# Performance work log

Measured on AMD Instinct MI355X. Metric: run time of the kernel, lower is better.

Reference implementation:

```python
import jax, jax.numpy as jnp
import numpy as np

N_NODES = 50000
N_EDGES = 640000
HID = 128
EDGE_FEAT = 4
NUM_G = 20
R_MIN, R_MAX = 0.0, 10.0

def setup_inputs() -> dict:
    key = jax.random.key(0)
    ks = jax.random.split(key, 16)
    s = lambda d: 1.0 / np.sqrt(d)
    return {
        'h': jax.random.normal(ks[0], (N_NODES, HID), jnp.float32),
        'x': jax.random.normal(ks[1], (N_NODES, 3), jnp.float32),
        'edge_index': jax.random.randint(ks[2], (2, N_EDGES), 0, N_NODES, dtype=jnp.int64),
        'mask_ligand': jnp.ones((N_NODES,), jnp.float32),
        'edge_attr': jax.random.normal(ks[3], (N_EDGES, EDGE_FEAT), jnp.float32),
        'We1': jax.random.normal(ks[4], (2*HID+EDGE_FEAT+NUM_G, HID), jnp.float32) * s(2*HID+EDGE_FEAT+NUM_G),
        'be1': jnp.zeros((HID,), jnp.float32),
        'We2': jax.random.normal(ks[5], (HID, HID), jnp.float32) * s(HID),
        'be2': jnp.zeros((HID,), jnp.float32),
        'Winf': jax.random.normal(ks[6], (HID, 1), jnp.float32) * s(HID),
        'binf': jnp.zeros((1,), jnp.float32),
        'Wx1': jax.random.normal(ks[7], (HID, HID), jnp.float32) * s(HID),
        'bx1': jnp.zeros((HID,), jnp.float32),
        'Wx2': jax.random.normal(ks[8], (HID, 1), jnp.float32) * 0.001 * s(HID),
        'Wn1': jax.random.normal(ks[9], (2*HID, HID), jnp.float32) * s(2*HID),
        'bn1': jnp.zeros((HID,), jnp.float32),
        'Wn2': jax.random.normal(ks[10], (HID, HID), jnp.float32) * s(HID),
        'bn2': jnp.zeros((HID,), jnp.float32),
    }

def reference(h, x, edge_index, mask_ligand, edge_attr,
              We1, be1, We2, be2, Winf, binf, Wx1, bx1, Wx2, Wn1, bn1, Wn2, bn2):
    n = h.shape[0]
    src, dst = edge_index[0], edge_index[1]
    hi, hj = h[dst], h[src]                      # [E, H] gathers
    rel_x = x[dst] - x[src]                      # [E, 3]
    d_sq = jnp.sum(rel_x**2, axis=-1, keepdims=True)  # [E, 1]
    d = jnp.sqrt(d_sq + 1e-8)
    # GaussianSmearing(r_min=0, r_max=10, num_gaussians=20)
    offset = jnp.linspace(R_MIN, R_MAX, NUM_G, dtype=h.dtype)
    coeff = -0.5 / (offset[1] - offset[0])**2
    d_feat = jnp.exp(coeff * (d - offset)**2)    # [E, 20]
    edge_feat = jnp.concatenate([d_feat, edge_attr], axis=-1)
    # edge MLP (2 layers, silu, act_last=True)
    z = jnp.concatenate([hi, hj, edge_feat], axis=-1)
    mij = jax.nn.silu(jax.nn.silu(z @ We1 + be1) @ We2 + be2)  # [E, H]
    eij = jax.nn.sigmoid(mij @ Winf + binf)      # [E, 1]
    mi = jax.ops.segment_sum(mij * eij, dst, num_segments=n)   # [N, H]
    # node MLP (2 layers, silu, no act on last)
    nz = jnp.concatenate([mi, h], axis=-1)
    h_out = h + (jax.nn.silu(nz @ Wn1 + bn1) @ Wn2 + bn2)
    # coordinate update
    xg = jnp.tanh(jax.nn.silu(mij @ Wx1 + bx1) @ Wx2)          # [E, 1]
    delta_x = jax.ops.segment_sum(rel_x / (d + 1.0) * xg, dst, num_segments=n)
    x_out = x + delta_x * mask_ligand[:, None]
    return h_out, x_out
```

## Files before the change

kernel.cpp:

```cpp
#include <hip/hip_runtime.h>
#include <math.h>

#define NN 50000
#define NE 640000
#define H 128
#define EPB 64
#define NPB 32
#define ZB 296
#define BB 136
#define KP1 288
#define NZB 264
#define NBPAD 50176
#define HISTB (NE / 256)
#define CONVB 464
#define ALLOCB (NBPAD / 256)
#define HCONVB 3125

typedef __attribute__((ext_vector_type(8))) unsigned short u16x8;
typedef __attribute__((ext_vector_type(8))) __bf16 bf16x8;
typedef __attribute__((ext_vector_type(2))) __bf16 bf16x2;
typedef __attribute__((ext_vector_type(4))) float f32x4;

__device__ __forceinline__ float frcp(float x) {
#if __has_builtin(__builtin_amdgcn_rcpf)
    return __builtin_amdgcn_rcpf(x);
#else
    return 1.0f / x;
#endif
}

__device__ __forceinline__ float silu_f(float v) {
    return v * frcp(1.0f + __expf(-v));
}

__device__ __forceinline__ float sigmoid_f(float v) {
    return frcp(1.0f + __expf(-v));
}

__device__ __forceinline__ float tanh_f(float v) {
    return 1.0f - 2.0f * frcp(1.0f + __expf(2.0f * v));
}

__device__ __forceinline__ unsigned short f2bf(float f) {
    unsigned int u = __builtin_bit_cast(unsigned int, f);
    u += 0x7FFFu + ((u >> 16) & 1u);
    return (unsigned short)(u >> 16);
}

__device__ __forceinline__ float bf2f(unsigned short s) {
    unsigned int u = ((unsigned int)s) << 16;
    return __builtin_bit_cast(float, u);
}

__device__ __forceinline__ unsigned int pkbf(float lo, float hi) {
#if __has_builtin(__builtin_amdgcn_cvt_pk_bf16_f32)
    bf16x2 v = __builtin_amdgcn_cvt_pk_bf16_f32(lo, hi);
    unsigned int r; __builtin_memcpy(&r, &v, 4); return r;
#else
    return (unsigned int)f2bf(lo) | ((unsigned int)f2bf(hi) << 16);
#endif
}

__device__ __forceinline__ f32x4 mfma16(u16x8 a, u16x8 b, f32x4 c) {
    return __builtin_amdgcn_mfma_f32_16x16x32_bf16(
        __builtin_bit_cast(bf16x8, a), __builtin_bit_cast(bf16x8, b), c, 0, 0, 0);
}

template<int KT, int INSTR, bool SYNC_BEFORE_EPI>
__device__ __forceinline__ void layer_mfma(
    const unsigned short* __restrict__ inbuf,
    const unsigned short* __restrict__ wt,
    const float* __restrict__ bias,
    unsigned short* __restrict__ outbuf,
    int wv, int quad, int r16)
{
    f32x4 acc[2][2] = {};
    const int F = wv * 32;
    #pragma unroll
    for (int ks = 0; ks < KT / 32; ks++) {
        int ko = ks * 32 + quad * 8;
        u16x8 b0 = *(const u16x8*)(inbuf + r16 * INSTR + ko);
        u16x8 b1 = *(const u16x8*)(inbuf + (16 + r16) * INSTR + ko);
        u16x8 a0 = *(const u16x8*)(wt + (size_t)(F + r16) * KT + ko);
        u16x8 a1 = *(const u16x8*)(wt + (size_t)(F + 16 + r16) * KT + ko);
        acc[0][0] = mfma16(a0, b0, acc[0][0]);
        acc[0][1] = mfma16(a0, b1, acc[0][1]);
        acc[1][0] = mfma16(a1, b0, acc[1][0]);
        acc[1][1] = mfma16(a1, b1, acc[1][1]);
    }
    if (SYNC_BEFORE_EPI) __syncthreads();
    #pragma unroll
    for (int rt = 0; rt < 2; rt++) {
        int f0 = F + rt * 16 + quad * 4;
        float4 bv = *(const float4*)(bias + f0);
        #pragma unroll
        for (int ci = 0; ci < 2; ci++) {
            int e = ci * 16 + r16;
            float s0 = silu_f(acc[rt][ci][0] + bv.x);
            float s1 = silu_f(acc[rt][ci][1] + bv.y);
            float s2 = silu_f(acc[rt][ci][2] + bv.z);
            float s3 = silu_f(acc[rt][ci][3] + bv.w);
            uint2 p = { pkbf(s0, s1), pkbf(s2, s3) };
            *(uint2*)(outbuf + e * BB + f0) = p;
        }
    }
}

__global__ __launch_bounds__(256) void init_kernel(
    float4* __restrict__ out4, int n4out,
    float4* __restrict__ ws4, int n4ws)
{
    int i = blockIdx.x * 256 + threadIdx.x;
    float4 z = make_float4(0.f, 0.f, 0.f, 0.f);
    if (i < n4out) out4[i] = z;
    else if (i - n4out < n4ws) ws4[i - n4out] = z;
}

__global__ __launch_bounds__(256) void hist_conv_kernel(
    const int* __restrict__ ei, int* __restrict__ cnt, int histBlocks,
    const float* __restrict__ We1, const float* __restrict__ We2,
    const float* __restrict__ Wx1, const float* __restrict__ Wn1,
    const float* __restrict__ Wn2,
    unsigned short* __restrict__ w1t, unsigned short* __restrict__ w2t,
    unsigned short* __restrict__ wx1t, unsigned short* __restrict__ wn1t,
    unsigned short* __restrict__ wn2t)
{
    int b = blockIdx.x, t = threadIdx.x;
    if (b < histBlocks) {
        int i = b * 256 + t;
        atomicAdd(&cnt[ei[NE + i]], 1);
        return;
    }
    int i = (b - histBlocks) * 256 + t;
    const int S1 = 128 * KP1;
    const int S2 = 128 * 128;
    const int S3 = 128 * 256;
    if (i < S1) {
        int n = i / KP1, k = i % KP1;
        w1t[i] = (k < 280) ? f2bf(We1[k * H + n]) : (unsigned short)0;
    } else if (i < S1 + S2) {
        int j = i - S1; int n = j / H, k = j % H;
        w2t[j] = f2bf(We2[k * H + n]);
    } else if (i < S1 + 2 * S2) {
        int j = i - S1 - S2; int n = j / H, k = j % H;
        wx1t[j] = f2bf(Wx1[k * H + n]);
    } else if (i < S1 + 2 * S2 + S3) {
        int j = i - S1 - 2 * S2; int n = j / 256, k = j % 256;
        wn1t[j] = f2bf(Wn1[k * H + n]);
    } else if (i < S1 + 3 * S2 + S3) {
        int j = i - S1 - 2 * S2 - S3; int n = j / H, k = j % H;
        wn2t[j] = f2bf(Wn2[k * H + n]);
    }
}

__global__ __launch_bounds__(256) void alloc_hconv_kernel(
    const int* __restrict__ cnt, int* __restrict__ cur, int* __restrict__ gtot,
    const float* __restrict__ h, unsigned short* __restrict__ hb,
    int allocBlocks)
{
    int b = blockIdx.x, t = threadIdx.x;
    if (b < allocBlocks) {
        int d = b * 256 + t;
        int v = cnt[d];
        int incl = v;
        #pragma unroll
        for (int o = 1; o < 64; o <<= 1) {
            int u = __shfl_up(incl, o, 64);
            if ((t & 63) >= o) incl += u;
        }
        int total = __shfl(incl, 63, 64);
        int base = 0;
        if ((t & 63) == 63) base = atomicAdd(gtot, total);
        base = __shfl(base, 63, 64);
        cur[d] = base + incl - v;
        return;
    }
    int j = (b - allocBlocks) * 256 + t;
    const float4* hp = (const float4*)h + (size_t)j * 2;
    float4 a = hp[0], c = hp[1];
    uint4 pk = { pkbf(a.x, a.y), pkbf(a.z, a.w), pkbf(c.x, c.y), pkbf(c.z, c.w) };
    ((uint4*)hb)[j] = pk;
}

__global__ __launch_bounds__(256) void scatter_kernel(
    const int* __restrict__ ei, const float* __restrict__ edge_attr,
    int* __restrict__ cur, uint4* __restrict__ epay)
{
    int i = blockIdx.x * 256 + threadIdx.x;
    int s = ei[i], d = ei[NE + i];
    float4 ea = ((const float4*)edge_attr)[i];
    int p = atomicAdd(&cur[d], 1);
    uint4 pv = { (unsigned)s, (unsigned)d, pkbf(ea.x, ea.y), pkbf(ea.z, ea.w) };
    epay[p] = pv;
}

__global__ __launch_bounds__(512, 6) void edge_kernel(
    const float* __restrict__ h, const float* __restrict__ x,
    const int* __restrict__ ei, const float* __restrict__ edge_attr,
    const unsigned short* __restrict__ w1t, const float* __restrict__ be1,
    const unsigned short* __restrict__ w2t, const float* __restrict__ be2,
    const float* __restrict__ Winf, const float* __restrict__ binf,
    const unsigned short* __restrict__ wx1t, const float* __restrict__ bx1,
    const float* __restrict__ Wx2,
    const uint4* __restrict__ epay, const unsigned short* __restrict__ hb,
    float* __restrict__ mi, float* __restrict__ dx)
{
    __shared__ unsigned short zs[EPB * ZB];
    __shared__ float relx_s[EPB][3];
    __shared__ float eij_s[EPB];
    __shared__ float xg_s[EPB];
    __shared__ float epart[8][EPB];
    __shared__ float xpart[8][EPB];
    __shared__ int dst_s[EPB];
    __shared__ float winf_s[H];
    __shared__ float wx2_s[H];

    unsigned short* m1 = zs;
    unsigned short* m2 = zs + EPB * BB;

    const int t = threadIdx.x;
    const int e0 = blockIdx.x * EPB;
    const bool srt = (epay != nullptr);

    if (t >= 128 && t < 256) {
        winf_s[t - 128] = Winf[t - 128];
        wx2_s[t - 128] = Wx2[t - 128];
    }

    {
        int e = t >> 3, l = t & 7;
        unsigned short* zr = zs + e * ZB;
        if (srt) {
            uint4 pv = epay[e0 + e];
            const uint4* hd = (const uint4*)(hb + (size_t)pv.y * H);
            const uint4* hs = (const uint4*)(hb + (size_t)pv.x * H);
            uint4 a0 = hd[l * 2], a1 = hd[l * 2 + 1];
            *(uint4*)(zr + l * 16) = a0;
            *(uint4*)(zr + l * 16 + 8) = a1;
            uint4 c0 = hs[l * 2], c1 = hs[l * 2 + 1];
            *(uint4*)(zr + 128 + l * 16) = c0;
            *(uint4*)(zr + 128 + l * 16 + 8) = c1;
        } else {
            int s = ei[e0 + e], d = ei[NE + e0 + e];
            const float4* hd = (const float4*)(h + (size_t)d * H);
            const float4* hs = (const float4*)(h + (size_t)s * H);
            float4 v0 = hd[l * 4 + 0], v1 = hd[l * 4 + 1];
            float4 v2 = hd[l * 4 + 2], v3 = hd[l * 4 + 3];
            uint4 p0 = { pkbf(v0.x, v0.y), pkbf(v0.z, v0.w), pkbf(v1.x, v1.y), pkbf(v1.z, v1.w) };
            uint4 p1 = { pkbf(v2.x, v2.y), pkbf(v2.z, v2.w), pkbf(v3.x, v3.y), pkbf(v3.z, v3.w) };
            *(uint4*)(zr + l * 16) = p0;
            *(uint4*)(zr + l * 16 + 8) = p1;
            float4 w0 = hs[l * 4 + 0], w1 = hs[l * 4 + 1];
            float4 w2 = hs[l * 4 + 2], w3 = hs[l * 4 + 3];
            uint4 q0 = { pkbf(w0.x, w0.y), pkbf(w0.z, w0.w), pkbf(w1.x, w1.y), pkbf(w1.z, w1.w) };
            uint4 q1 = { pkbf(w2.x, w2.y), pkbf(w2.z, w2.w), pkbf(w3.x, w3.y), pkbf(w3.z, w3.w) };
            *(uint4*)(zr + 128 + l * 16) = q0;
            *(uint4*)(zr + 128 + l * 16 + 8) = q1;
        }
    }
    if (t < EPB) {
        unsigned short* zr = zs + t * ZB;
        int s, d;
        if (srt) {
            uint4 pv = epay[e0 + t];
            s = (int)pv.x; d = (int)pv.y;
            *(unsigned int*)(zr + 276) = pv.z;
            *(unsigned int*)(zr + 278) = pv.w;
        } else {
            s = ei[e0 + t]; d = ei[NE + e0 + t];
            #pragma unroll
            for (int j = 0; j < 4; j++)
                zr[276 + j] = f2bf(edge_attr[(size_t)(e0 + t) * 4 + j]);
        }
        dst_s[t] = d;
        float rx = x[d * 3 + 0] - x[s * 3 + 0];
        float ry = x[d * 3 + 1] - x[s * 3 + 1];
        float rz = x[d * 3 + 2] - x[s * 3 + 2];
        float d2 = rx * rx + ry * ry + rz * rz;
        float dd = sqrtf(d2 + 1e-8f);
        float inv = frcp(dd + 1.0f);
        relx_s[t][0] = rx * inv;
        relx_s[t][1] = ry * inv;
        relx_s[t][2] = rz * inv;
        const float step = 10.0f / 19.0f;
        const float coeff = -0.5f / (step * step);
        #pragma unroll
        for (int g = 0; g < 20; g++) {
            float df = dd - step * (float)g;
            zr[256 + g] = f2bf(__expf(coeff * df * df));
        }
        #pragma unroll
        for (int j = 280; j < ZB; j++) zr[j] = 0;
    }
    __syncthreads();

    const int wv = t >> 6, lane = t & 63;
    const int quad = lane >> 4, r16 = lane & 15;
    const int F = wv * 16;
    const int f0 = F + quad * 4;

    {
        f32x4 acc[4] = {};
        #pragma unroll
        for (int ks = 0; ks < KP1 / 32; ks++) {
            int ko = ks * 32 + quad * 8;
            u16x8 a = *(const u16x8*)(w1t + (size_t)(F + r16) * KP1 + ko);
            #pragma unroll
            for (int ci = 0; ci < 4; ci++) {
                u16x8 b = *(const u16x8*)(zs + (ci * 16 + r16) * ZB + ko);
                acc[ci] = mfma16(a, b, acc[ci]);
            }
        }
        __syncthreads();
        float4 bv = *(const float4*)(be1 + f0);
        #pragma unroll
        for (int ci = 0; ci < 4; ci++) {
            int e = ci * 16 + r16;
            float s0 = silu_f(acc[ci][0] + bv.x);
            float s1 = silu_f(acc[ci][1] + bv.y);
            float s2 = silu_f(acc[ci][2] + bv.z);
            float s3 = silu_f(acc[ci][3] + bv.w);
            uint2 p = { pkbf(s0, s1), pkbf(s2, s3) };
            *(uint2*)(m1 + e * BB + f0) = p;
        }
    }
    __syncthreads();

    {
        f32x4 acc[4] = {};
        #pragma unroll
        for (int ks = 0; ks < H / 32; ks++) {
            int ko = ks * 32 + quad * 8;
            u16x8 a = *(const u16x8*)(w2t + (size_t)(F + r16) * H + ko);
            #pragma unroll
            for (int ci = 0; ci < 4; ci++) {
                u16x8 b = *(const u16x8*)(m1 + (ci * 16 + r16) * BB + ko);
                acc[ci] = mfma16(a, b, acc[ci]);
            }
        }
        float4 bv = *(const float4*)(be2 + f0);
        float4 wf = *(const float4*)(winf_s + f0);
        float ep[4];
        #pragma unroll
        for (int ci = 0; ci < 4; ci++) {
            int e = ci * 16 + r16;
            float s0 = silu_f(acc[ci][0] + bv.x);
            float s1 = silu_f(acc[ci][1] + bv.y);
            float s2 = silu_f(acc[ci][2] + bv.z);
            float s3 = silu_f(acc[ci][3] + bv.w);
            ep[ci] = s0 * wf.x + s1 * wf.y + s2 * wf.z + s3 * wf.w;
            uint2 p = { pkbf(s0, s1), pkbf(s2, s3) };
            *(uint2*)(m2 + e * BB + f0) = p;
        }
        #pragma unroll
        for (int ci = 0; ci < 4; ci++) {
            ep[ci] += __shfl_xor(ep[ci], 16, 64);
            ep[ci] += __shfl_xor(ep[ci], 32, 64);
        }
        if (quad == 0) {
            #pragma unroll
            for (int ci = 0; ci < 4; ci++)
                epart[wv][ci * 16 + r16] = ep[ci];
        }
    }
    __syncthreads();

    if (t < EPB) {
        float s = binf[0];
        #pragma unroll
        for (int w = 0; w < 8; w++) s += epart[w][t];
        eij_s[t] = sigmoid_f(s);
    }

    {
        f32x4 acc[4] = {};
        #pragma unroll
        for (int ks = 0; ks < H / 32; ks++) {
            int ko = ks * 32 + quad * 8;
            u16x8 a = *(const u16x8*)(wx1t + (size_t)(F + r16) * H + ko);
            #pragma unroll
            for (int ci = 0; ci < 4; ci++) {
                u16x8 b = *(const u16x8*)(m2 + (ci * 16 + r16) * BB + ko);
                acc[ci] = mfma16(a, b, acc[ci]);
            }
        }
        float4 bv = *(const float4*)(bx1 + f0);
        float4 wf = *(const float4*)(wx2_s + f0);
        float xp[4];
        #pragma unroll
        for (int ci = 0; ci < 4; ci++) {
            xp[ci] = silu_f(acc[ci][0] + bv.x) * wf.x
                   + silu_f(acc[ci][1] + bv.y) * wf.y
                   + silu_f(acc[ci][2] + bv.z) * wf.z
                   + silu_f(acc[ci][3] + bv.w) * wf.w;
        }
        #pragma unroll
        for (int ci = 0; ci < 4; ci++) {
            xp[ci] += __shfl_xor(xp[ci], 16, 64);
            xp[ci] += __shfl_xor(xp[ci], 32, 64);
        }
        if (quad == 0) {
            #pragma unroll
            for (int ci = 0; ci < 4; ci++)
                xpart[wv][ci * 16 + r16] = xp[ci];
        }
    }
    __syncthreads();

    if (t < EPB) {
        float xs = 0.f;
        #pragma unroll
        for (int w = 0; w < 8; w++) xs += xpart[w][t];
        xg_s[t] = tanh_f(xs);
    }
    __syncthreads();

    if (t < 128) {
        const int k = t;
        float acc = 0.f;
        int rs = 0;
        #pragma unroll
        for (int c = 0; c < EPB; c += 8) {
            float v[8];
            #pragma unroll
            for (int j = 0; j < 8; j++)
                v[j] = bf2f(m2[(c + j) * BB + k]) * eij_s[c + j];
            #pragma unroll
            for (int j = 0; j < 8; j++) {
                int e = c + j;
                acc += v[j];
                if (e == EPB - 1 || dst_s[e + 1] != dst_s[e]) {
                    float* p = &mi[(size_t)dst_s[e] * H + k];
                    if (srt && rs > 0 && e < EPB - 1) *p = acc;
                    else atomicAdd(p, acc);
                    acc = 0.f;
                    rs = e + 1;
                }
            }
        }
    } else if (t < 131) {
        const int dd = t - 128;
        float acc = 0.f;
        int rs = 0;
        #pragma unroll
        for (int c = 0; c < EPB; c += 8) {
            float v[8];
            #pragma unroll
            for (int j = 0; j < 8; j++)
                v[j] = relx_s[c + j][dd] * xg_s[c + j];
            #pragma unroll
            for (int j = 0; j < 8; j++) {
                int e = c + j;
                acc += v[j];
                if (e == EPB - 1 || dst_s[e + 1] != dst_s[e]) {
                    float* p = &dx[(size_t)dst_s[e] * 3 + dd];
                    if (srt && rs > 0 && e < EPB - 1) *p = acc;
                    else atomicAdd(p, acc);
                    acc = 0.f;
                    rs = e + 1;
                }
            }
        }
    }
}

__global__ __launch_bounds__(256, 8) void node_kernel(
    const float* __restrict__ h, const float* __restrict__ x,
    const float* __restrict__ mask,
    const unsigned short* __restrict__ wn1t, const float* __restrict__ bn1,
    const unsigned short* __restrict__ wn2t, const float* __restrict__ bn2,
    float* __restrict__ mi_hout, float* __restrict__ dx_xout)
{
    __shared__ unsigned short nzs[NPB * NZB];

    unsigned short* nbuf = nzs;

    const int t = threadIdx.x;
    const int n0 = blockIdx.x * NPB;

    {
        int r = t >> 3, l = t & 7;
        int n = n0 + r;
        unsigned short* zr = nzs + r * NZB;
        if (n < NN) {
            const float4* mi4 = (const float4*)(mi_hout + (size_t)n * H);
            const float4* h4  = (const float4*)(h + (size_t)n * H);
            float4 v0 = mi4[l * 4 + 0], v1 = mi4[l * 4 + 1];
            float4 v2 = mi4[l * 4 + 2], v3 = mi4[l * 4 + 3];
            uint4 p0 = { pkbf(v0.x, v0.y), pkbf(v0.z, v0.w), pkbf(v1.x, v1.y), pkbf(v1.z, v1.w) };
            uint4 p1 = { pkbf(v2.x, v2.y), pkbf(v2.z, v2.w), pkbf(v3.x, v3.y), pkbf(v3.z, v3.w) };
            *(uint4*)(zr + l * 16) = p0;
            *(uint4*)(zr + l * 16 + 8) = p1;
            float4 w0 = h4[l * 4 + 0], w1 = h4[l * 4 + 1];
            float4 w2 = h4[l * 4 + 2], w3 = h4[l * 4 + 3];
            uint4 q0 = { pkbf(w0.x, w0.y), pkbf(w0.z, w0.w), pkbf(w1.x, w1.y), pkbf(w1.z, w1.w) };
            uint4 q1 = { pkbf(w2.x, w2.y), pkbf(w2.z, w2.w), pkbf(w3.x, w3.y), pkbf(w3.z, w3.w) };
            *(uint4*)(zr + 128 + l * 16) = q0;
            *(uint4*)(zr + 128 + l * 16 + 8) = q1;
        } else {
            uint4 zf = {0u, 0u, 0u, 0u};
            *(uint4*)(zr + l * 16) = zf;
            *(uint4*)(zr + l * 16 + 8) = zf;
            *(uint4*)(zr + 128 + l * 16) = zf;
            *(uint4*)(zr + 128 + l * 16 + 8) = zf;
        }
    }

    float xo = 0.f;
    int xn = -1, xdim = 0;
    if (t < NPB * 3) {
        int r = t / 3; xdim = t % 3;
        int n = n0 + r;
        if (n < NN) {
            xn = n;
            xo = x[(size_t)n * 3 + xdim] + dx_xout[(size_t)n * 3 + xdim] * mask[n];
        }
    }
    __syncthreads();

    if (xn >= 0) dx_xout[(size_t)xn * 3 + xdim] = xo;

    const int wv = t >> 6, lane = t & 63;
    const int quad = lane >> 4, r16 = lane & 15;

    layer_mfma<2 * H, NZB, true>(nzs, wn1t, bn1, nbuf, wv, quad, r16);
    __syncthreads();

    {
        f32x4 acc[2][2] = {};
        const int F = wv * 32;
        #pragma unroll
        for (int ks = 0; ks < H / 32; ks++) {
            int ko = ks * 32 + quad * 8;
            u16x8 b0 = *(const u16x8*)(nbuf + r16 * BB + ko);
            u16x8 b1 = *(const u16x8*)(nbuf + (16 + r16) * BB + ko);
            u16x8 a0 = *(const u16x8*)(wn2t + (size_t)(F + r16) * H + ko);
            u16x8 a1 = *(const u16x8*)(wn2t + (size_t)(F + 16 + r16) * H + ko);
            acc[0][0] = mfma16(a0, b0, acc[0][0]);
            acc[0][1] = mfma16(a0, b1, acc[0][1]);
            acc[1][0] = mfma16(a1, b0, acc[1][0]);
            acc[1][1] = mfma16(a1, b1, acc[1][1]);
        }
        #pragma unroll
        for (int rt = 0; rt < 2; rt++) {
            int f0 = F + rt * 16 + quad * 4;
            float4 bv = *(const float4*)(bn2 + f0);
            #pragma unroll
            for (int ci = 0; ci < 2; ci++) {
                int n = n0 + ci * 16 + r16;
                if (n < NN) {
                    float4 hv = *(const float4*)(h + (size_t)n * H + f0);
                    float4 o;
                    o.x = hv.x + acc[rt][ci][0] + bv.x;
                    o.y = hv.y + acc[rt][ci][1] + bv.y;
                    o.z = hv.z + acc[rt][ci][2] + bv.z;
                    o.w = hv.w + acc[rt][ci][3] + bv.w;
                    *(float4*)(mi_hout + (size_t)n * H + f0) = o;
                }
            }
        }
    }
}

extern "C" void kernel_launch(void* const* d_in, const int* in_sizes, int n_in,
                              void* d_out, int out_size, void* d_ws, size_t ws_size,
                              hipStream_t stream) {
    const float* h     = (const float*)d_in[0];
    const float* x     = (const float*)d_in[1];
    const int*   ei    = (const int*)d_in[2];
    const float* mask  = (const float*)d_in[3];
    const float* eattr = (const float*)d_in[4];
    const float* We1   = (const float*)d_in[5];
    const float* be1   = (const float*)d_in[6];
    const float* We2   = (const float*)d_in[7];
    const float* be2   = (const float*)d_in[8];
    const float* Winf  = (const float*)d_in[9];
    const float* binf  = (const float*)d_in[10];
    const float* Wx1   = (const float*)d_in[11];
    const float* bx1   = (const float*)d_in[12];
    const float* Wx2   = (const float*)d_in[13];
    const float* Wn1   = (const float*)d_in[14];
    const float* bn1   = (const float*)d_in[15];
    const float* Wn2   = (const float*)d_in[16];
    const float* bn2   = (const float*)d_in[17];

    float* mi = (float*)d_out;
    float* dx = mi + (size_t)NN * H;

    char* wsb  = (char*)d_ws;
    unsigned short* w1t  = (unsigned short*)wsb;
    unsigned short* w2t  = w1t + 128 * KP1;
    unsigned short* wx1t = w2t + 128 * H;
    unsigned short* wn1t = wx1t + 128 * H;
    unsigned short* wn2t = wn1t + 128 * 256;

    const size_t OFF_CNT  = 262144;
    const size_t OFF_CUR  = OFF_CNT + (size_t)NBPAD * 4;
    const size_t OFF_GTOT = OFF_CUR + (size_t)NBPAD * 4;
    const size_t OFF_HB   = OFF_GTOT + 16;
    const size_t OFF_EPAY = OFF_HB + (size_t)NN * H * 2;
    const size_t WS_NEED  = OFF_EPAY + (size_t)NE * 16;

    int*   cnt  = (int*)(wsb + OFF_CNT);
    int*   cur  = (int*)(wsb + OFF_CUR);
    int*   gtot = (int*)(wsb + OFF_GTOT);
    unsigned short* hb = (unsigned short*)(wsb + OFF_HB);
    uint4* epay = (uint4*)(wsb + OFF_EPAY);

    const bool full = (ws_size >= WS_NEED);

    const int n4out = (NN * H + NN * 3) / 4;
    const int n4ws  = full ? (int)((OFF_HB - OFF_CNT) / 16) : 0;
    init_kernel<<<(n4out + n4ws + 255) / 256, 256, 0, stream>>>(
        (float4*)d_out, n4out, (float4*)(wsb + OFF_CNT), n4ws);

    {
        int hb_ = full ? HISTB : 0;
        hist_conv_kernel<<<hb_ + CONVB, 256, 0, stream>>>(
            ei, cnt, hb_, We1, We2, Wx1, Wn1, Wn2, w1t, w2t, wx1t, wn1t, wn2t);
    }

    if (full) {
        alloc_hconv_kernel<<<ALLOCB + HCONVB, 256, 0, stream>>>(
            cnt, cur, gtot, h, hb, ALLOCB);
        scatter_kernel<<<NE / 256, 256, 0, stream>>>(ei, eattr, cur, epay);
    }

    edge_kernel<<<NE / EPB, 512, 0, stream>>>(
        h, x, ei, eattr, w1t, be1, w2t, be2, Winf, binf, wx1t, bx1, Wx2,
        full ? epay : (const uint4*)nullptr,
        full ? hb : (const unsigned short*)nullptr,
        mi, dx);

    node_kernel<<<(NN + NPB - 1) / NPB, 256, 0, stream>>>(
        h, x, mask, wn1t, bn1, wn2t, bn2, mi, dx);
}
```

Measured before the change: 433.8 us.

## Shrink edge LDS, use atomic reductions, widen node kernel and reuse bf16 h

New measurement: 449.9 us. 1.04x slower.

```diff
diff --git a/kernel.cpp b/kernel.cpp
--- a/kernel.cpp
+++ b/kernel.cpp
@@ -5,8 +5,8 @@
 #define NE 640000
 #define H 128
 #define EPB 64
-#define NPB 32
-#define ZB 296
+#define NPB 64
+#define ZB 280
 #define BB 136
 #define KP1 288
 #define NZB 264
@@ -64,46 +64,6 @@
 __device__ __forceinline__ f32x4 mfma16(u16x8 a, u16x8 b, f32x4 c) {
     return __builtin_amdgcn_mfma_f32_16x16x32_bf16(
         __builtin_bit_cast(bf16x8, a), __builtin_bit_cast(bf16x8, b), c, 0, 0, 0);
-}
-
-template<int KT, int INSTR, bool SYNC_BEFORE_EPI>
-__device__ __forceinline__ void layer_mfma(
-    const unsigned short* __restrict__ inbuf,
-    const unsigned short* __restrict__ wt,
-    const float* __restrict__ bias,
-    unsigned short* __restrict__ outbuf,
-    int wv, int quad, int r16)
-{
-    f32x4 acc[2][2] = {};
-    const int F = wv * 32;
-    #pragma unroll
-    for (int ks = 0; ks < KT / 32; ks++) {
-        int ko = ks * 32 + quad * 8;
-        u16x8 b0 = *(const u16x8*)(inbuf + r16 * INSTR + ko);
-        u16x8 b1 = *(const u16x8*)(inbuf + (16 + r16) * INSTR + ko);
-        u16x8 a0 = *(const u16x8*)(wt + (size_t)(F + r16) * KT + ko);
-        u16x8 a1 = *(const u16x8*)(wt + (size_t)(F + 16 + r16) * KT + ko);
-        acc[0][0] = mfma16(a0, b0, acc[0][0]);
-        acc[0][1] = mfma16(a0, b1, acc[0][1]);
-        acc[1][0] = mfma16(a1, b0, acc[1][0]);
-        acc[1][1] = mfma16(a1, b1, acc[1][1]);
-    }
-    if (SYNC_BEFORE_EPI) __syncthreads();
-    #pragma unroll
-    for (int rt = 0; rt < 2; rt++) {
-        int f0 = F + rt * 16 + quad * 4;
-        float4 bv = *(const float4*)(bias + f0);
-        #pragma unroll
-        for (int ci = 0; ci < 2; ci++) {
-            int e = ci * 16 + r16;
-            float s0 = silu_f(acc[rt][ci][0] + bv.x);
-            float s1 = silu_f(acc[rt][ci][1] + bv.y);
-            float s2 = silu_f(acc[rt][ci][2] + bv.z);
-            float s3 = silu_f(acc[rt][ci][3] + bv.w);
-            uint2 p = { pkbf(s0, s1), pkbf(s2, s3) };
-            *(uint2*)(outbuf + e * BB + f0) = p;
-        }
-    }
 }
 
 __global__ __launch_bounds__(256) void init_kernel(
@@ -194,7 +154,7 @@
     epay[p] = pv;
 }
 
-__global__ __launch_bounds__(512, 6) void edge_kernel(
+__global__ __launch_bounds__(512, 8) void edge_kernel(
     const float* __restrict__ h, const float* __restrict__ x,
     const int* __restrict__ ei, const float* __restrict__ edge_attr,
     const unsigned short* __restrict__ w1t, const float* __restrict__ be1,
@@ -205,12 +165,10 @@
     const uint4* __restrict__ epay, const unsigned short* __restrict__ hb,
     float* __restrict__ mi, float* __restrict__ dx)
 {
-    __shared__ unsigned short zs[EPB * ZB];
+    __shared__ unsigned short zs[EPB * ZB + 8];
     __shared__ float relx_s[EPB][3];
-    __shared__ float eij_s[EPB];
-    __shared__ float xg_s[EPB];
-    __shared__ float epart[8][EPB];
-    __shared__ float xpart[8][EPB];
+    __shared__ float eij_acc[EPB];
+    __shared__ float xg_acc[EPB];
     __shared__ int dst_s[EPB];
     __shared__ float winf_s[H];
     __shared__ float wx2_s[H];
@@ -225,6 +183,12 @@
     if (t >= 128 && t < 256) {
         winf_s[t - 128] = Winf[t - 128];
         wx2_s[t - 128] = Wx2[t - 128];
+    } else if (t >= 256 && t < 320) {
+        eij_acc[t - 256] = binf[0];
+        xg_acc[t - 256] = 0.f;
+    } else if (t == 320) {
+        uint4 zf = {0u, 0u, 0u, 0u};
+        *(uint4*)(zs + EPB * ZB) = zf;
     }
 
     {
@@ -289,8 +253,6 @@
             float df = dd - step * (float)g;
             zr[256 + g] = f2bf(__expf(coeff * df * df));
         }
-        #pragma unroll
-        for (int j = 280; j < ZB; j++) zr[j] = 0;
     }
     __syncthreads();
 
@@ -360,17 +322,12 @@
         if (quad == 0) {
             #pragma unroll
             for (int ci = 0; ci < 4; ci++)
-                epart[wv][ci * 16 + r16] = ep[ci];
+                atomicAdd(&eij_acc[ci * 16 + r16], ep[ci]);
         }
     }
     __syncthreads();
 
-    if (t < EPB) {
-        float s = binf[0];
-        #pragma unroll
-        for (int w = 0; w < 8; w++) s += epart[w][t];
-        eij_s[t] = sigmoid_f(s);
-    }
+    if (t < EPB) eij_acc[t] = sigmoid_f(eij_acc[t]);
 
     {
         f32x4 acc[4] = {};
@@ -402,17 +359,12 @@
         if (quad == 0) {
             #pragma unroll
             for (int ci = 0; ci < 4; ci++)
-                xpart[wv][ci * 16 + r16] = xp[ci];
+                atomicAdd(&xg_acc[ci * 16 + r16], xp[ci]);
         }
     }
     __syncthreads();
 
-    if (t < EPB) {
-        float xs = 0.f;
-        #pragma unroll
-        for (int w = 0; w < 8; w++) xs += xpart[w][t];
-        xg_s[t] = tanh_f(xs);
-    }
+    if (t < EPB) xg_acc[t] = tanh_f(xg_acc[t]);
     __syncthreads();
 
     if (t < 128) {
@@ -424,7 +376,7 @@
             float v[8];
             #pragma unroll
             for (int j = 0; j < 8; j++)
-                v[j] = bf2f(m2[(c + j) * BB + k]) * eij_s[c + j];
+                v[j] = bf2f(m2[(c + j) * BB + k]) * eij_acc[c + j];
             #pragma unroll
             for (int j = 0; j < 8; j++) {
                 int e = c + j;
@@ -447,7 +399,7 @@
             float v[8];
             #pragma unroll
             for (int j = 0; j < 8; j++)
-                v[j] = relx_s[c + j][dd] * xg_s[c + j];
+                v[j] = relx_s[c + j][dd] * xg_acc[c + j];
             #pragma unroll
             for (int j = 0; j < 8; j++) {
                 int e = c + j;
@@ -464,11 +416,12 @@
     }
 }
 
-__global__ __launch_bounds__(256, 8) void node_kernel(
+__global__ __launch_bounds__(512, 8) void node_kernel(
     const float* __restrict__ h, const float* __restrict__ x,
     const float* __restrict__ mask,
     const unsigned short* __restrict__ wn1t, const float* __restrict__ bn1,
     const unsigned short* __restrict__ wn2t, const float* __restrict__ bn2,
+    const unsigned short* __restrict__ hb,
     float* __restrict__ mi_hout, float* __restrict__ dx_xout)
 {
     __shared__ unsigned short nzs[NPB * NZB];
@@ -484,19 +437,25 @@
         unsigned short* zr = nzs + r * NZB;
         if (n < NN) {
             const float4* mi4 = (const float4*)(mi_hout + (size_t)n * H);
-            const float4* h4  = (const float4*)(h + (size_t)n * H);
             float4 v0 = mi4[l * 4 + 0], v1 = mi4[l * 4 + 1];
             float4 v2 = mi4[l * 4 + 2], v3 = mi4[l * 4 + 3];
             uint4 p0 = { pkbf(v0.x, v0.y), pkbf(v0.z, v0.w), pkbf(v1.x, v1.y), pkbf(v1.z, v1.w) };
             uint4 p1 = { pkbf(v2.x, v2.y), pkbf(v2.z, v2.w), pkbf(v3.x, v3.y), pkbf(v3.z, v3.w) };
             *(uint4*)(zr + l * 16) = p0;
             *(uint4*)(zr + l * 16 + 8) = p1;
-            float4 w0 = h4[l * 4 + 0], w1 = h4[l * 4 + 1];
-            float4 w2 = h4[l * 4 + 2], w3 = h4[l * 4 + 3];
-            uint4 q0 = { pkbf(w0.x, w0.y), pkbf(w0.z, w0.w), pkbf(w1.x, w1.y), pkbf(w1.z, w1.w) };
-            uint4 q1 = { pkbf(w2.x, w2.y), pkbf(w2.z, w2.w), pkbf(w3.x, w3.y), pkbf(w3.z, w3.w) };
-            *(uint4*)(zr + 128 + l * 16) = q0;
-            *(uint4*)(zr + 128 + l * 16 + 8) = q1;
+            if (hb) {
+                const uint4* hs = (const uint4*)(hb + (size_t)n * H);
+                *(uint4*)(zr + 128 + l * 16) = hs[l * 2];
+                *(uint4*)(zr + 128 + l * 16 + 8) = hs[l * 2 + 1];
+            } else {
+                const float4* h4 = (const float4*)(h + (size_t)n * H);
+                float4 w0 = h4[l * 4 + 0], w1 = h4[l * 4 + 1];
+                float4 w2 = h4[l * 4 + 2], w3 = h4[l * 4 + 3];
+                uint4 q0 = { pkbf(w0.x, w0.y), pkbf(w0.z, w0.w), pkbf(w1.x, w1.y), pkbf(w1.z, w1.w) };
+                uint4 q1 = { pkbf(w2.x, w2.y), pkbf(w2.z, w2.w), pkbf(w3.x, w3.y), pkbf(w3.z, w3.w) };
+                *(uint4*)(zr + 128 + l * 16) = q0;
+                *(uint4*)(zr + 128 + l * 16 + 8) = q1;
+            }
         } else {
             uint4 zf = {0u, 0u, 0u, 0u};
             *(uint4*)(zr + l * 16) = zf;
@@ -522,41 +481,60 @@
 
     const int wv = t >> 6, lane = t & 63;
     const int quad = lane >> 4, r16 = lane & 15;
-
-    layer_mfma<2 * H, NZB, true>(nzs, wn1t, bn1, nbuf, wv, quad, r16);
+    const int F = wv * 16;
+    const int f0 = F + quad * 4;
+
+    {
+        f32x4 acc[4] = {};
+        #pragma unroll
+        for (int ks = 0; ks < 2 * H / 32; ks++) {
+            int ko = ks * 32 + quad * 8;
+            u16x8 a = *(const u16x8*)(wn1t + (size_t)(F + r16) * (2 * H) + ko);
+            #pragma unroll
+            for (int ci = 0; ci < 4; ci++) {
+                u16x8 b = *(const u16x8*)(nzs + (ci * 16 + r16) * NZB + ko);
+                acc[ci] = mfma16(a, b, acc[ci]);
+            }
+        }
+        __syncthreads();
+        float4 bv = *(const float4*)(bn1 + f0);
+        #pragma unroll
+        for (int ci = 0; ci < 4; ci++) {
+            int e = ci * 16 + r16;
+            float s0 = silu_f(acc[ci][0] + bv.x);
+            float s1 = silu_f(acc[ci][1] + bv.y);
+            float s2 = silu_f(acc[ci][2] + bv.z);
+            float s3 = silu_f(acc[ci][3] + bv.w);
+            uint2 p = { pkbf(s0, s1), pkbf(s2, s3) };
+            *(uint2*)(nbuf + e * BB + f0) = p;
+        }
+    }
     __syncthreads();
 
     {
-        f32x4 acc[2][2] = {};
-        const int F = wv * 32;
+        f32x4 acc[4] = {};
         #pragma unroll
         for (int ks = 0; ks < H / 32; ks++) {
             int ko = ks * 32 + quad * 8;
-            u16x8 b0 = *(const u16x8*)(nbuf + r16 * BB + ko);
-            u16x8 b1 = *(const u16x8*)(nbuf + (16 + r16) * BB + ko);
-            u16x8 a0 = *(const u16x8*)(wn2t + (size_t)(F + r16) * H + ko);
-            u16x8 a1 = *(const u16x8*)(wn2t + (size_t)(F + 16 + r16) * H + ko);
-            acc[0][0] = mfma16(a0, b0, acc[0][0]);
-            acc[0][1] = mfma16(a0, b1, acc[0][1]);
-            acc[1][0] = mfma16(a1, b0, acc[1][0]);
-            acc[1][1] = mfma16(a1, b1, acc[1][1]);
-        }
-        #pragma unroll
-        for (int rt = 0; rt < 2; rt++) {
-            int f0 = F + rt * 16 + quad * 4;
-            float4 bv = *(const float4*)(bn2 + f0);
-            #pragma unroll
-            for (int ci = 0; ci < 2; ci++) {
-                int n = n0 + ci * 16 + r16;
-                if (n < NN) {
-                    float4 hv = *(const float4*)(h + (size_t)n * H + f0);
-                    float4 o;
-                    o.x = hv.x + acc[rt][ci][0] + bv.x;
-                    o.y = hv.y + acc[rt][ci][1] + bv.y;
-                    o.z = hv.z + acc[rt][ci][2] + bv.z;
-                    o.w = hv.w + acc[rt][ci][3] + bv.w;
-                    *(float4*)(mi_hout + (size_t)n * H + f0) = o;
-                }
+            u16x8 a = *(const u16x8*)(wn2t + (size_t)(F + r16) * H + ko);
+            #pragma unroll
+            for (int ci = 0; ci < 4; ci++) {
+                u16x8 b = *(const u16x8*)(nbuf + (ci * 16 + r16) * BB + ko);
+                acc[ci] = mfma16(a, b, acc[ci]);
+            }
+        }
+        float4 bv = *(const float4*)(bn2 + f0);
+        #pragma unroll
+        for (int ci = 0; ci < 4; ci++) {
+            int n = n0 + ci * 16 + r16;
+            if (n < NN) {
+                float4 hv = *(const float4*)(h + (size_t)n * H + f0);
+                float4 o;
+                o.x = hv.x + acc[ci][0] + bv.x;
+                o.y = hv.y + acc[ci][1] + bv.y;
+                o.z = hv.z + acc[ci][2] + bv.z;
+                o.w = hv.w + acc[ci][3] + bv.w;
+                *(float4*)(mi_hout + (size_t)n * H + f0) = o;
             }
         }
     }
@@ -595,22 +573,22 @@
     unsigned short* wn2t = wn1t + 128 * 256;
 
     const size_t OFF_CNT  = 262144;
-    const size_t OFF_CUR  = OFF_CNT + (size_t)NBPAD * 4;
-    const size_t OFF_GTOT = OFF_CUR + (size_t)NBPAD * 4;
-    const size_t OFF_HB   = OFF_GTOT + 16;
+    const size_t OFF_GTOT = OFF_CNT + (size_t)NBPAD * 4;
+    const size_t OFF_CUR  = OFF_GTOT + 16;
+    const size_t OFF_HB   = OFF_CUR + (size_t)NBPAD * 4;
     const size_t OFF_EPAY = OFF_HB + (size_t)NN * H * 2;
     const size_t WS_NEED  = OFF_EPAY + (size_t)NE * 16;
 
     int*   cnt  = (int*)(wsb + OFF_CNT);
+    int*   gtot = (int*)(wsb + OFF_GTOT);
     int*   cur  = (int*)(wsb + OFF_CUR);
-    int*   gtot = (int*)(wsb + OFF_GTOT);
     unsigned short* hb = (unsigned short*)(wsb + OFF_HB);
     uint4* epay = (uint4*)(wsb + OFF_EPAY);
 
     const bool full = (ws_size >= WS_NEED);
 
     const int n4out = (NN * H + NN * 3) / 4;
-    const int n4ws  = full ? (int)((OFF_HB - OFF_CNT) / 16) : 0;
+    const int n4ws  = full ? (int)((OFF_CUR - OFF_CNT) / 16) : 0;
     init_kernel<<<(n4out + n4ws + 255) / 256, 256, 0, stream>>>(
         (float4*)d_out, n4out, (float4*)(wsb + OFF_CNT), n4ws);
 
@@ -632,6 +610,8 @@
         full ? hb : (const unsigned short*)nullptr,
         mi, dx);
 
-    node_kernel<<<(NN + NPB - 1) / NPB, 256, 0, stream>>>(
-        h, x, mask, wn1t, bn1, wn2t, bn2, mi, dx);
-}
+    node_kernel<<<(NN + NPB - 1) / NPB, 512, 0, stream>>>(
+        h, x, mask, wn1t, bn1, wn2t, bn2,
+        full ? hb : (const unsigned short*)nullptr,
+        mi, dx);
+}
```
